# Optimization experiments

Measured on AMD Instinct MI355X. Metric: run time of the kernel, lower is better.

The kernel has to match this reference:

```python
import jax, jax.numpy as jnp
import numpy as np

DIM = 768
NUM_HEADS = 12
HEAD_DIM = DIM // NUM_HEADS
SCALE = HEAD_DIM ** -0.5


def setup_inputs() -> dict:
    key = jax.random.key(0)
    k1, k2, k3, k4, k5 = jax.random.split(key, 5)
    B, N = 1, 4096
    x = jax.random.normal(k1, (B, N, DIM), dtype=jnp.float32)
    xpos = jax.random.randint(k2, (B, N, 2), 0, 64, dtype=jnp.int64)
    # learned parameters (torch nn.Linear convention: W is [out, in])
    W_qkv = jax.random.normal(k3, (3 * DIM, DIM), dtype=jnp.float32) * 0.02
    W_proj = jax.random.normal(k4, (DIM, DIM), dtype=jnp.float32) * 0.02
    b_proj = jax.random.normal(k5, (DIM,), dtype=jnp.float32) * 0.02
    return {"x": x, "xpos": xpos, "W_qkv": W_qkv, "W_proj": W_proj, "b_proj": b_proj}


def reference(x, xpos, W_qkv, W_proj, b_proj):
    B, N, C = x.shape
    H, D = NUM_HEADS, HEAD_DIM
    # qkv projection (no bias), then split into q,k,v of shape [B,H,N,D]
    qkv = jnp.einsum('bnc,fc->bnf', x, W_qkv)            # [B,N,3C]
    qkv = qkv.reshape(B, N, 3, H, D).transpose(2, 0, 3, 1, 4)  # [3,B,H,N,D]
    q, k, v = qkv[0], qkv[1], qkv[2]
    # rope is None in this config -> q,k unchanged; xpos unused
    attn = jnp.einsum('bhnd,bhmd->bhnm', q, k) * SCALE   # [B,H,N,N]
    attn = jax.nn.softmax(attn, axis=-1)
    out = jnp.einsum('bhnm,bhmd->bhnd', attn, v)          # [B,H,N,D]
    out = out.transpose(0, 2, 1, 3).reshape(B, N, C)      # [B,N,C]
    out = jnp.einsum('bnc,oc->bno', out, W_proj) + b_proj
    return out
```

## Files before the change

### kernel.cpp

```cpp
#include <hip/hip_runtime.h>

#define DEVI __device__ __forceinline__

typedef unsigned short u16;
typedef unsigned int u32;
using u16x8 = __attribute__((ext_vector_type(8))) u16;
using u16x4 = __attribute__((ext_vector_type(4))) u16;
using u32x4 = __attribute__((ext_vector_type(4))) u32;
using bf16x8 = __attribute__((ext_vector_type(8))) __bf16;
using f32x4 = __attribute__((ext_vector_type(4))) float;
using f32x16 = __attribute__((ext_vector_type(16))) float;

typedef const __attribute__((address_space(1))) u32 gu32;
typedef __attribute__((address_space(3))) u32 lu32;

#if __has_builtin(__builtin_amdgcn_exp2f)
#define EXP2(x) __builtin_amdgcn_exp2f(x)
#else
#define EXP2(x) __builtin_exp2f(x)
#endif

DEVI u16 f2bf(float f) {
    u32 u = __builtin_bit_cast(u32, f);
    u32 r = (u + 0x7fffu + ((u >> 16) & 1u)) >> 16;
    return (u16)r;
}
DEVI float bf2f(u16 b) {
    u32 u = ((u32)b) << 16;
    return __builtin_bit_cast(float, u);
}
DEVI u32 cvtpk_bf16(float lo, float hi) {
    u32 r;
    asm("v_cvt_pk_bf16_f32 %0, %1, %2" : "=v"(r) : "v"(lo), "v"(hi));
    return r;
}

DEVI bf16x8 frag_ld(const u16* p) {
    return __builtin_bit_cast(bf16x8, *(const u16x8*)p);
}

DEVI void async16(const void* g, void* lds) {
    __builtin_amdgcn_global_load_lds((gu32*)g, (lu32*)lds, 16, 0, 0);
}

#define MFMA32(a, b, c) __builtin_amdgcn_mfma_f32_32x32x16_bf16(a, b, c, 0, 0, 0)

#define QK_SCALE 0.18033688011112042f

__global__ void cvt3_kernel(const float* __restrict__ s0, const float* __restrict__ s1,
                            const float* __restrict__ s2,
                            u16* __restrict__ d0, u16* __restrict__ d1, u16* __restrict__ d2,
                            int n0, int n1) {
    int i = (blockIdx.x * blockDim.x + threadIdx.x) * 4;
    const float* s; u16* d;
    if (i < n0) { s = s0; d = d0; }
    else if (i < n0 + n1) { s = s1 - n0; d = d1 - n0; }
    else { s = s2 - (n0 + n1); d = d2 - (n0 + n1); }
    float4 v = *(const float4*)(s + i);
    u16x4 o;
    o[0] = f2bf(v.x); o[1] = f2bf(v.y); o[2] = f2bf(v.z); o[3] = f2bf(v.w);
    *(u16x4*)(d + i) = o;
}

template<int MODE>
__global__ __launch_bounds__(256) void gemm_bt(const u16* __restrict__ A,
                                               const u16* __restrict__ B,
                                               void* __restrict__ Out,
                                               const float* __restrict__ bias,
                                               int M, int Nn, int K) {
    const int m0 = blockIdx.x * 128, n0 = blockIdx.y * 128;
    const int tid = threadIdx.x, w = tid >> 6, lane = tid & 63;
    const int l15 = lane & 15, l4 = lane >> 4;
    __shared__ __align__(16) u16 As[128 * 32];
    __shared__ __align__(16) u16 Bs[128 * 32];
    const int wm = (w >> 1) * 64, wn = (w & 1) * 64;
    f32x4 acc[4][4] = {};
    const int srow = lane >> 2;
    const int sk = (lane & 3) * 8;

    for (int kt = 0; kt < K; kt += 32) {
#pragma unroll
        for (int it = 0; it < 2; ++it) {
            const int rbase = (w * 2 + it) * 16;
            async16(A + (size_t)(m0 + rbase + srow) * K + kt + sk, &As[rbase * 32]);
            async16(B + (size_t)(n0 + rbase + srow) * K + kt + sk, &Bs[rbase * 32]);
        }
        __syncthreads();
        bf16x8 af[4], bfr[4];
#pragma unroll
        for (int i = 0; i < 4; ++i) {
            af[i] = frag_ld(&As[(wm + i * 16 + l15) * 32 + l4 * 8]);
            bfr[i] = frag_ld(&Bs[(wn + i * 16 + l15) * 32 + l4 * 8]);
        }
#pragma unroll
        for (int i = 0; i < 4; ++i)
#pragma unroll
            for (int j = 0; j < 4; ++j)
                acc[i][j] = __builtin_amdgcn_mfma_f32_16x16x32_bf16(af[i], bfr[j], acc[i][j], 0, 0, 0);
        __syncthreads();
    }
#pragma unroll
    for (int i = 0; i < 4; ++i)
#pragma unroll
        for (int j = 0; j < 4; ++j)
#pragma unroll
            for (int r = 0; r < 4; ++r) {
                const int row = m0 + wm + i * 16 + l4 * 4 + r;
                const int col = n0 + wn + j * 16 + l15;
                if (MODE == 0) {
                    float v = acc[i][j][r];
                    if (col < 768) v *= QK_SCALE;
                    ((u16*)Out)[(size_t)row * Nn + col] = f2bf(v);
                } else {
                    ((float*)Out)[(size_t)row * Nn + col] = acc[i][j][r] + bias[col];
                }
            }
}

__global__ __launch_bounds__(256) void pack_kv(const u16* __restrict__ qkv,
                                               u16* __restrict__ kt,
                                               u16* __restrict__ vt2) {
    const int sb = blockIdx.x;
    const int h = blockIdx.y;
    const int tid = threadIdx.x;
    __shared__ u16 T[64][72];
#pragma unroll
    for (int rd = 0; rd < 2; ++rd) {
        const int idx = rd * 256 + tid;
        const int row = idx >> 3, ch = idx & 7;
        u16x8 v = *(const u16x8*)(qkv + (size_t)(sb * 64 + row) * 2304 + 1536 + h * 64 + ch * 8);
        *(u16x8*)&T[row][ch * 8] = v;
    }
#pragma unroll
    for (int rd = 0; rd < 2; ++rd) {
        const int o = rd * 256 + tid;
        const int s_loc = o >> 8, mm = (o >> 6) & 3, lane = o & 63;
        const int l31 = lane & 31, hi = lane >> 5;
        u16x8 kv = *(const u16x8*)(qkv + (size_t)(sb * 64 + s_loc * 32 + l31) * 2304 +
                                   768 + h * 64 + mm * 16 + hi * 8);
        const int s = sb * 2 + s_loc;
        *(u16x8*)(kt + ((size_t)(h * 128 + s) * 4 + mm) * 512 + lane * 8) = kv;
    }
    __syncthreads();
#pragma unroll
    for (int rd = 0; rd < 2; ++rd) {
        const int o = rd * 256 + tid;
        const int s_loc = o >> 8, f = (o >> 6) & 3, lane = o & 63;
        const int ks = f >> 1, Oh = f & 1;
        const int l31 = lane & 31, hi = lane >> 5;
        u16x8 ov;
#pragma unroll
        for (int j = 0; j < 8; ++j) {
            const int kvloc = 32 * s_loc + 16 * ks + (j & 3) + 8 * (j >> 2) + 4 * hi;
            ov[j] = T[kvloc][Oh * 32 + l31];
        }
        const int s = sb * 2 + s_loc;
        *(u16x8*)(vt2 + ((size_t)(h * 128 + s) * 4 + f) * 512 + lane * 8) = ov;
    }
}

__global__ __launch_bounds__(128, 2) void attn_kernel(const u16* __restrict__ qkv,
                                                      const u16* __restrict__ kt,
                                                      const u16* __restrict__ vt2,
                                                      u16* __restrict__ op,
                                                      float* __restrict__ lsums) {
    const int id = blockIdx.x;
    const int xcd = id & 7, slot = id >> 3;
    const int gi = slot >> 5, qbi = slot & 31;
    const int g = gi * 8 + xcd;
    const int h = g % 12, sp = g / 12;
    const int tid = threadIdx.x, w = tid >> 6, lane = tid & 63;
    const int l31 = lane & 31, hi = lane >> 5;
    const int q0 = qbi * 128 + w * 64;

    bf16x8 qA0, qA1, qA2, qA3, qB0, qB1, qB2, qB3;
    {
        const u16* qp = qkv + (size_t)(q0 + l31) * 2304 + h * 64 + hi * 8;
        qA0 = frag_ld(qp); qA1 = frag_ld(qp + 16);
        qA2 = frag_ld(qp + 32); qA3 = frag_ld(qp + 48);
        const u16* qp2 = qp + (size_t)32 * 2304;
        qB0 = frag_ld(qp2); qB1 = frag_ld(qp2 + 16);
        qB2 = frag_ld(qp2 + 32); qB3 = frag_ld(qp2 + 48);
    }

    const u16* kc = kt + (size_t)(h * 128 + sp * 32) * 2048 + lane * 8;
    const u16* vc = vt2 + (size_t)(h * 128 + sp * 32) * 2048 + lane * 8;

    f32x16 O0 = {}, O1 = {}, O2 = {}, O3 = {};
    float lsumA = 0.f, lsumB = 0.f;

    bf16x8 kf0 = frag_ld(kc), kf1 = frag_ld(kc + 512),
           kf2 = frag_ld(kc + 1024), kf3 = frag_ld(kc + 1536);
    bf16x8 vf0 = frag_ld(vc), vf1 = frag_ld(vc + 512),
           vf2 = frag_ld(vc + 1024), vf3 = frag_ld(vc + 1536);
    kc += 2048; vc += 2048;

#pragma unroll 1
    for (int s = 0; s < 32; ++s) {
        f32x16 S0 = {}, S1 = {};
        __builtin_amdgcn_s_setprio(1);
        S0 = MFMA32(kf0, qA0, S0);  S1 = MFMA32(kf0, qB0, S1);
        S0 = MFMA32(kf1, qA1, S0);  S1 = MFMA32(kf1, qB1, S1);
        S0 = MFMA32(kf2, qA2, S0);  S1 = MFMA32(kf2, qB2, S1);
        S0 = MFMA32(kf3, qA3, S0);  S1 = MFMA32(kf3, qB3, S1);
        __builtin_amdgcn_s_setprio(0);
        kf0 = frag_ld(kc); kf1 = frag_ld(kc + 512);
        kf2 = frag_ld(kc + 1024); kf3 = frag_ld(kc + 1536);
        kc += 2048;

        float e[16], f[16];
#pragma unroll
        for (int r = 0; r < 16; ++r) e[r] = EXP2(S0[r]);
#pragma unroll
        for (int r = 0; r < 16; ++r) f[r] = EXP2(S1[r]);
        u32x4 wa0 = { cvtpk_bf16(e[0], e[1]), cvtpk_bf16(e[2], e[3]),
                      cvtpk_bf16(e[4], e[5]), cvtpk_bf16(e[6], e[7]) };
        u32x4 wa1 = { cvtpk_bf16(e[8], e[9]), cvtpk_bf16(e[10], e[11]),
                      cvtpk_bf16(e[12], e[13]), cvtpk_bf16(e[14], e[15]) };
        u32x4 wb0 = { cvtpk_bf16(f[0], f[1]), cvtpk_bf16(f[2], f[3]),
                      cvtpk_bf16(f[4], f[5]), cvtpk_bf16(f[6], f[7]) };
        u32x4 wb1 = { cvtpk_bf16(f[8], f[9]), cvtpk_bf16(f[10], f[11]),
                      cvtpk_bf16(f[12], f[13]), cvtpk_bf16(f[14], f[15]) };
        bf16x8 pasA0 = __builtin_bit_cast(bf16x8, wa0);
        bf16x8 pasA1 = __builtin_bit_cast(bf16x8, wa1);
        bf16x8 pasB0 = __builtin_bit_cast(bf16x8, wb0);
        bf16x8 pasB1 = __builtin_bit_cast(bf16x8, wb1);
        lsumA += ((((e[0] + e[1]) + (e[2] + e[3])) +
                   ((e[4] + e[5]) + (e[6] + e[7]))) +
                  (((e[8] + e[9]) + (e[10] + e[11])) +
                   ((e[12] + e[13]) + (e[14] + e[15]))));
        lsumB += ((((f[0] + f[1]) + (f[2] + f[3])) +
                   ((f[4] + f[5]) + (f[6] + f[7]))) +
                  (((f[8] + f[9]) + (f[10] + f[11])) +
                   ((f[12] + f[13]) + (f[14] + f[15]))));

        __builtin_amdgcn_s_setprio(1);
        O0 = MFMA32(pasA0, vf0, O0);  O2 = MFMA32(pasB0, vf0, O2);
        O1 = MFMA32(pasA0, vf1, O1);  O3 = MFMA32(pasB0, vf1, O3);
        O0 = MFMA32(pasA1, vf2, O0);  O2 = MFMA32(pasB1, vf2, O2);
        O1 = MFMA32(pasA1, vf3, O1);  O3 = MFMA32(pasB1, vf3, O3);
        __builtin_amdgcn_s_setprio(0);
        vf0 = frag_ld(vc); vf1 = frag_ld(vc + 512);
        vf2 = frag_ld(vc + 1024); vf3 = frag_ld(vc + 1536);
        vc += 2048;
    }

    lsumA += __shfl_xor(lsumA, 32);
    lsumB += __shfl_xor(lsumB, 32);
    u16* ob = op + (size_t)sp * 3145728;
    const int rr4 = 4 * hi;
#pragma unroll
    for (int r = 0; r < 16; ++r) {
        const int q = (r & 3) + 8 * (r >> 2) + rr4;
        const size_t rowoff = (size_t)(q0 + q) * 768 + h * 64 + l31;
        ob[rowoff] = f2bf(O0[r]);
        ob[rowoff + 32] = f2bf(O1[r]);
        const size_t rowoff2 = rowoff + (size_t)32 * 768;
        ob[rowoff2] = f2bf(O2[r]);
        ob[rowoff2 + 32] = f2bf(O3[r]);
    }
    if (hi == 0) {
        lsums[(size_t)sp * 49152 + (size_t)(q0 + l31) * 12 + h] = lsumA;
        lsums[(size_t)sp * 49152 + (size_t)(q0 + 32 + l31) * 12 + h] = lsumB;
    }
}

__global__ __launch_bounds__(256) void combine_kernel(const u16* __restrict__ op,
                                                      const float* __restrict__ lsums,
                                                      u16* __restrict__ outb) {
    const int gid = blockIdx.x * 256 + threadIdx.x;
    const int e = gid * 8;
    const int q = e / 768, c = e % 768, h = c >> 6;
    float lt = 0.f;
#pragma unroll
    for (int sp = 0; sp < 4; ++sp) lt += lsums[(size_t)sp * 49152 + q * 12 + h];
    const float inv = 1.0f / lt;
    float acc[8] = {};
#pragma unroll
    for (int sp = 0; sp < 4; ++sp) {
        u16x8 o = *(const u16x8*)(op + (size_t)sp * 3145728 + (size_t)q * 768 + c);
#pragma unroll
        for (int jj = 0; jj < 8; ++jj) acc[jj] += bf2f(o[jj]);
    }
    u16x8 o;
#pragma unroll
    for (int jj = 0; jj < 8; ++jj) o[jj] = f2bf(acc[jj] * inv);
    *(u16x8*)(outb + e) = o;
}

extern "C" void kernel_launch(void* const* d_in, const int* in_sizes, int n_in,
                              void* d_out, int out_size, void* d_ws, size_t ws_size,
                              hipStream_t stream) {
    const float* x = (const float*)d_in[0];
    const float* Wqkv = (const float*)d_in[2];
    const float* Wproj = (const float*)d_in[3];
    const float* bproj = (const float*)d_in[4];

    u16* ws = (u16*)d_ws;
    u16* x_bf = ws;
    u16* wqkv_bf = x_bf + 3145728;
    u16* wproj_bf = wqkv_bf + 1769472;
    u16* qkv = wproj_bf + 589824;
    u16* attn_bf = qkv + 9437184;
    u16* vt2 = attn_bf + 3145728;
    u16* o_part = vt2 + 3145728;
    float* lsums = (float*)(o_part + 12582912);
    u16* kt = x_bf;

    cvt3_kernel<<<5376, 256, 0, stream>>>(x, Wqkv, Wproj, x_bf, wqkv_bf, wproj_bf,
                                          3145728, 1769472);

    gemm_bt<0><<<dim3(32, 18), 256, 0, stream>>>(x_bf, wqkv_bf, qkv, nullptr, 4096, 2304, 768);
    pack_kv<<<dim3(64, 12), 256, 0, stream>>>(qkv, kt, vt2);
    attn_kernel<<<1536, 128, 0, stream>>>(qkv, kt, vt2, o_part, lsums);
    combine_kernel<<<1536, 256, 0, stream>>>(o_part, lsums, attn_bf);
    gemm_bt<1><<<dim3(32, 6), 256, 0, stream>>>(attn_bf, wproj_bf, d_out, bproj, 4096, 768, 768);
}
```

Before: 127.8 us.

## Read K directly from qkv buffer and halve attention KV splits

Drops the K repacking pass and has the attention kernel load K fragments straight from the row-major qkv buffer with per-row strided loads. The KV split factor goes from 4 to 2, so each block runs twice as many KV steps, the grid halves, and the combine kernel reads only two partial outputs and sums. This is meant to cut the packing kernel's traffic and the partial-output write/read volume. The cost is less coalesced K loads and fewer blocks, which may leave CUs underused or uneven across waves.

```diff
diff --git a/kernel.cpp b/kernel.cpp
--- a/kernel.cpp
+++ b/kernel.cpp
@@ -117,9 +117,8 @@
             }
 }
 
-__global__ __launch_bounds__(256) void pack_kv(const u16* __restrict__ qkv,
-                                               u16* __restrict__ kt,
-                                               u16* __restrict__ vt2) {
+__global__ __launch_bounds__(256) void pack_v(const u16* __restrict__ qkv,
+                                              u16* __restrict__ vt2) {
     const int sb = blockIdx.x;
     const int h = blockIdx.y;
     const int tid = threadIdx.x;
@@ -130,16 +129,6 @@
         const int row = idx >> 3, ch = idx & 7;
         u16x8 v = *(const u16x8*)(qkv + (size_t)(sb * 64 + row) * 2304 + 1536 + h * 64 + ch * 8);
         *(u16x8*)&T[row][ch * 8] = v;
-    }
-#pragma unroll
-    for (int rd = 0; rd < 2; ++rd) {
-        const int o = rd * 256 + tid;
-        const int s_loc = o >> 8, mm = (o >> 6) & 3, lane = o & 63;
-        const int l31 = lane & 31, hi = lane >> 5;
-        u16x8 kv = *(const u16x8*)(qkv + (size_t)(sb * 64 + s_loc * 32 + l31) * 2304 +
-                                   768 + h * 64 + mm * 16 + hi * 8);
-        const int s = sb * 2 + s_loc;
-        *(u16x8*)(kt + ((size_t)(h * 128 + s) * 4 + mm) * 512 + lane * 8) = kv;
     }
     __syncthreads();
 #pragma unroll
@@ -160,7 +149,6 @@
 }
 
 __global__ __launch_bounds__(128, 2) void attn_kernel(const u16* __restrict__ qkv,
-                                                      const u16* __restrict__ kt,
                                                       const u16* __restrict__ vt2,
                                                       u16* __restrict__ op,
                                                       float* __restrict__ lsums) {
@@ -183,20 +171,20 @@
         qB2 = frag_ld(qp2 + 32); qB3 = frag_ld(qp2 + 48);
     }
 
-    const u16* kc = kt + (size_t)(h * 128 + sp * 32) * 2048 + lane * 8;
-    const u16* vc = vt2 + (size_t)(h * 128 + sp * 32) * 2048 + lane * 8;
+    const u16* kc = qkv + (size_t)(sp * 2048 + l31) * 2304 + 768 + h * 64 + hi * 8;
+    const u16* vc = vt2 + (size_t)(h * 128 + sp * 64) * 2048 + lane * 8;
 
     f32x16 O0 = {}, O1 = {}, O2 = {}, O3 = {};
     float lsumA = 0.f, lsumB = 0.f;
 
-    bf16x8 kf0 = frag_ld(kc), kf1 = frag_ld(kc + 512),
-           kf2 = frag_ld(kc + 1024), kf3 = frag_ld(kc + 1536);
+    bf16x8 kf0 = frag_ld(kc), kf1 = frag_ld(kc + 16),
+           kf2 = frag_ld(kc + 32), kf3 = frag_ld(kc + 48);
     bf16x8 vf0 = frag_ld(vc), vf1 = frag_ld(vc + 512),
            vf2 = frag_ld(vc + 1024), vf3 = frag_ld(vc + 1536);
-    kc += 2048; vc += 2048;
+    kc += (size_t)32 * 2304; vc += 2048;
 
 #pragma unroll 1
-    for (int s = 0; s < 32; ++s) {
+    for (int s = 0; s < 64; ++s) {
         f32x16 S0 = {}, S1 = {};
         __builtin_amdgcn_s_setprio(1);
         S0 = MFMA32(kf0, qA0, S0);  S1 = MFMA32(kf0, qB0, S1);
@@ -204,9 +192,9 @@
         S0 = MFMA32(kf2, qA2, S0);  S1 = MFMA32(kf2, qB2, S1);
         S0 = MFMA32(kf3, qA3, S0);  S1 = MFMA32(kf3, qB3, S1);
         __builtin_amdgcn_s_setprio(0);
-        kf0 = frag_ld(kc); kf1 = frag_ld(kc + 512);
-        kf2 = frag_ld(kc + 1024); kf3 = frag_ld(kc + 1536);
-        kc += 2048;
+        kf0 = frag_ld(kc); kf1 = frag_ld(kc + 16);
+        kf2 = frag_ld(kc + 32); kf3 = frag_ld(kc + 48);
+        kc += (size_t)32 * 2304;
 
         float e[16], f[16];
 #pragma unroll
@@ -271,20 +259,14 @@
     const int gid = blockIdx.x * 256 + threadIdx.x;
     const int e = gid * 8;
     const int q = e / 768, c = e % 768, h = c >> 6;
-    float lt = 0.f;
-#pragma unroll
-    for (int sp = 0; sp < 4; ++sp) lt += lsums[(size_t)sp * 49152 + q * 12 + h];
+    float lt = lsums[q * 12 + h] + lsums[49152 + q * 12 + h];
     const float inv = 1.0f / lt;
-    float acc[8] = {};
-#pragma unroll
-    for (int sp = 0; sp < 4; ++sp) {
-        u16x8 o = *(const u16x8*)(op + (size_t)sp * 3145728 + (size_t)q * 768 + c);
-#pragma unroll
-        for (int jj = 0; jj < 8; ++jj) acc[jj] += bf2f(o[jj]);
-    }
+    u16x8 o1 = *(const u16x8*)(op + (size_t)q * 768 + c);
+    u16x8 o2 = *(const u16x8*)(op + 3145728 + (size_t)q * 768 + c);
     u16x8 o;
 #pragma unroll
-    for (int jj = 0; jj < 8; ++jj) o[jj] = f2bf(acc[jj] * inv);
+    for (int jj = 0; jj < 8; ++jj)
+        o[jj] = f2bf((bf2f(o1[jj]) + bf2f(o2[jj])) * inv);
     *(u16x8*)(outb + e) = o;
 }
 
@@ -304,15 +286,14 @@
     u16* attn_bf = qkv + 9437184;
     u16* vt2 = attn_bf + 3145728;
     u16* o_part = vt2 + 3145728;
-    float* lsums = (float*)(o_part + 12582912);
-    u16* kt = x_bf;
+    float* lsums = (float*)(o_part + 6291456);
 
     cvt3_kernel<<<5376, 256, 0, stream>>>(x, Wqkv, Wproj, x_bf, wqkv_bf, wproj_bf,
                                           3145728, 1769472);
 
     gemm_bt<0><<<dim3(32, 18), 256, 0, stream>>>(x_bf, wqkv_bf, qkv, nullptr, 4096, 2304, 768);
-    pack_kv<<<dim3(64, 12), 256, 0, stream>>>(qkv, kt, vt2);
-    attn_kernel<<<1536, 128, 0, stream>>>(qkv, kt, vt2, o_part, lsums);
+    pack_v<<<dim3(64, 12), 256, 0, stream>>>(qkv, vt2);
+    attn_kernel<<<768, 128, 0, stream>>>(qkv, vt2, o_part, lsums);
     combine_kernel<<<1536, 256, 0, stream>>>(o_part, lsums, attn_bf);
     gemm_bt<1><<<dim3(32, 6), 256, 0, stream>>>(attn_bf, wproj_bf, d_out, bproj, 4096, 768, 768);
 }
```

Result: no change. 127.0 us (-0.6%).
